# Kernel optimization log

Hardware: AMD Instinct MI355X
Metric: run time of the kernel (lower is better)

## Reference

```python
import jax, jax.numpy as jnp
import numpy as np

N_NODES = 50000
N_EDGES = 800000
NUM_GRAPHS = 256
EPS = 1e-5


def _gcn_conv(x, edge_index, W, b):
    # PyG GCNConv: add self-loops, sym-normalize, aggregate, then add bias.
    n = x.shape[0]
    xw = x @ W  # [N, out]
    loops = jnp.arange(n)
    row = jnp.concatenate([edge_index[0], loops])  # source
    col = jnp.concatenate([edge_index[1], loops])  # target
    deg = jax.ops.segment_sum(jnp.ones_like(col, dtype=xw.dtype), col, num_segments=n)
    dinv = jnp.where(deg > 0, jax.lax.rsqrt(deg), 0.0)
    norm = dinv[row] * dinv[col]  # [E+N]
    msg = norm[:, None] * xw[row]  # gather + scale
    out = jax.ops.segment_sum(msg, col, num_segments=n)  # scatter-add
    return out + b


def _bn(x, g, b, m, v):
    # inference-mode batch norm
    return (x - m) * jax.lax.rsqrt(v + EPS) * g + b


def reference(x, edge_index, batch, gcn_W0, gcn_b0, bn_g0, bn_b0, bn_m0, bn_v0,
              gcn_W1, gcn_b1, bn_g1, bn_b1, bn_m1, bn_v1,
              hW1, hb1, hg1, hbb1, hm1, hv1,
              hW2, hb2, hg2, hbb2, hm2, hv2,
              hW3, hb3, hW4, hb4):
    # GCN block 0
    h = _gcn_conv(x, edge_index, gcn_W0, gcn_b0)
    h = jax.nn.relu(_bn(h, bn_g0, bn_b0, bn_m0, bn_v0))  # dropout = identity (eval)
    # GCN block 1
    h = _gcn_conv(h, edge_index, gcn_W1, gcn_b1)
    h = jax.nn.relu(_bn(h, bn_g1, bn_b1, bn_m1, bn_v1))
    # global mean pool over graphs
    sums = jax.ops.segment_sum(h, batch, num_segments=NUM_GRAPHS)
    cnts = jax.ops.segment_sum(jnp.ones_like(batch, dtype=h.dtype), batch, num_segments=NUM_GRAPHS)
    pooled = sums / jnp.maximum(cnts, 1.0)[:, None]  # [G, 64]
    # MLP head (eval: dropout identity)
    z = jax.nn.relu(_bn(pooled @ hW1 + hb1, hg1, hbb1, hm1, hv1))
    z = jax.nn.relu(_bn(z @ hW2 + hb2, hg2, hbb2, hm2, hv2))
    z = jax.nn.relu(z @ hW3 + hb3)
    out = (z @ hW4 + hb4).reshape(-1)  # [G]
    return out


def setup_inputs() -> dict:
    key = jax.random.key(0)
    ks = jax.random.split(key, 12)
    d = 64
    inp = {
        'x': jax.random.normal(ks[0], (N_NODES, d), dtype=jnp.float32),
        'edge_index': jax.random.randint(ks[1], (2, N_EDGES), 0, N_NODES, dtype=jnp.int64),
        'batch': jnp.sort(jax.random.randint(ks[2], (N_NODES,), 0, NUM_GRAPHS, dtype=jnp.int64)),
        'gcn_W0': jax.random.normal(ks[3], (d, d), dtype=jnp.float32) * 0.1,
        'gcn_b0': jnp.zeros((d,), jnp.float32),
        'bn_g0': jnp.ones((d,), jnp.float32), 'bn_b0': jnp.zeros((d,), jnp.float32),
        'bn_m0': jnp.zeros((d,), jnp.float32), 'bn_v0': jnp.ones((d,), jnp.float32),
        'gcn_W1': jax.random.normal(ks[4], (d, d), dtype=jnp.float32) * 0.1,
        'gcn_b1': jnp.zeros((d,), jnp.float32),
        'bn_g1': jnp.ones((d,), jnp.float32), 'bn_b1': jnp.zeros((d,), jnp.float32),
        'bn_m1': jnp.zeros((d,), jnp.float32), 'bn_v1': jnp.ones((d,), jnp.float32),
        'hW1': jax.random.normal(ks[5], (d, 256), dtype=jnp.float32) * 0.1,
        'hb1': jnp.zeros((256,), jnp.float32),
        'hg1': jnp.ones((256,), jnp.float32), 'hbb1': jnp.zeros((256,), jnp.float32),
        'hm1': jnp.zeros((256,), jnp.float32), 'hv1': jnp.ones((256,), jnp.float32),
        'hW2': jax.random.normal(ks[6], (256, 128), dtype=jnp.float32) * 0.1,
        'hb2': jnp.zeros((128,), jnp.float32),
        'hg2': jnp.ones((128,), jnp.float32), 'hbb2': jnp.zeros((128,), jnp.float32),
        'hm2': jnp.zeros((128,), jnp.float32), 'hv2': jnp.ones((128,), jnp.float32),
        'hW3': jax.random.normal(ks[7], (128, 64), dtype=jnp.float32) * 0.1,
        'hb3': jnp.zeros((64,), jnp.float32),
        'hW4': jax.random.normal(ks[8], (64, 1), dtype=jnp.float32) * 0.1,
        'hb4': jnp.zeros((1,), jnp.float32),
    }
    return inp
```

## Files before the change

kernel.cpp:

```cpp
#include <hip/hip_runtime.h>
#include <hip/hip_bf16.h>
#include <hip/hip_fp16.h>

#define N_NODES 50000
#define N_EDGES 800000
#define NUM_GRAPHS 256
#define D 64
#define EPS 1e-5f
#define N_PART 8
#define PART_SIZE (N_NODES / N_PART)
#define SCAT_CHUNKS 512
#define WP 72

typedef _Float16 half8_t __attribute__((ext_vector_type(8)));
typedef float f32x4 __attribute__((ext_vector_type(4)));

__global__ __launch_bounds__(256) void scatter_cnt_kernel(
        const int* __restrict__ ei, int* __restrict__ cnt,
        unsigned short* __restrict__ ssrc, int cap, int E) {
    int p     = blockIdx.x & (N_PART - 1);
    int chunk = blockIdx.x >> 3;
    int per   = (E + SCAT_CHUNKS - 1) / SCAT_CHUNKS;
    int lo    = chunk * per;
    int hi    = lo + per; if (hi > E) hi = E;
    for (int e = lo + threadIdx.x; e < hi; e += 256) {
        int c = ei[E + e];
        if (c / PART_SIZE == p) {
            int r = ei[e];
            int pos = atomicAdd(&cnt[c], 1);
            if (pos < cap) ssrc[(size_t)c * cap + pos] = (unsigned short)r;
        }
    }
}

__global__ __launch_bounds__(256) void gemm64_kernel(const float* __restrict__ X,
                                                     const float* __restrict__ W,
                                                     const int* __restrict__ cnt,
                                                     __half* __restrict__ Yh, int N) {
    __shared__ _Float16 Xs[64 * WP];
    __shared__ _Float16 Wt[64 * WP];
    int tid  = threadIdx.x;
    int base = blockIdx.x * 64;
    for (int i = tid; i < 4096; i += 256) {
        int k = i >> 6, n = i & 63;
        Wt[n * WP + k] = (_Float16)W[i];
    }
    for (int i = tid; i < 1024; i += 256) {
        int r = i >> 4, c4 = (i & 15) * 4;
        float4 xv = (base + r < N)
            ? ((const float4*)X)[(size_t)(base + r) * 16 + (i & 15)]
            : make_float4(0.f, 0.f, 0.f, 0.f);
        _Float16* dst = &Xs[r * WP + c4];
        dst[0] = (_Float16)xv.x; dst[1] = (_Float16)xv.y;
        dst[2] = (_Float16)xv.z; dst[3] = (_Float16)xv.w;
    }
    __syncthreads();
    int wave  = tid >> 6;
    int lane  = tid & 63;
    int m     = lane & 15;
    int q     = lane >> 4;
    int row16 = wave * 16;
    half8_t a0 = *(const half8_t*)&Xs[(row16 + m) * WP + q * 8];
    half8_t a1 = *(const half8_t*)&Xs[(row16 + m) * WP + 32 + q * 8];
    f32x4 acc[4];
#pragma unroll
    for (int ct = 0; ct < 4; ct++) {
        half8_t b0 = *(const half8_t*)&Wt[(ct * 16 + m) * WP + q * 8];
        half8_t b1 = *(const half8_t*)&Wt[(ct * 16 + m) * WP + 32 + q * 8];
        f32x4 c = {0.f, 0.f, 0.f, 0.f};
        c = __builtin_amdgcn_mfma_f32_16x16x32_f16(a0, b0, c, 0, 0, 0);
        c = __builtin_amdgcn_mfma_f32_16x16x32_f16(a1, b1, c, 0, 0, 0);
        acc[ct] = c;
    }
    int   rows[4];
    float ws[4];
#pragma unroll
    for (int reg = 0; reg < 4; reg++) {
        rows[reg] = base + row16 + q * 4 + reg;
        ws[reg] = (rows[reg] < N) ? rsqrtf((float)cnt[rows[reg]] + 1.0f) : 0.0f;
    }
#pragma unroll
    for (int ct = 0; ct < 4; ct++) {
#pragma unroll
        for (int reg = 0; reg < 4; reg++) {
            if (rows[reg] < N)
                Yh[(size_t)rows[reg] * 64 + ct * 16 + m] =
                    (__half)(ws[reg] * acc[ct][reg]);
        }
    }
}

__device__ __forceinline__ void acc_row(uint4 v, float4& A, float4& B) {
    __half2* hp = (__half2*)&v;
    float2 q0 = __half22float2(hp[0]), q1 = __half22float2(hp[1]);
    float2 q2 = __half22float2(hp[2]), q3 = __half22float2(hp[3]);
    A.x += q0.x; A.y += q0.y; A.z += q1.x; A.w += q1.y;
    B.x += q2.x; B.y += q2.y; B.z += q3.x; B.w += q3.y;
}

__global__ __launch_bounds__(256) void agg_bn_kernel(
        const __half* __restrict__ xwh, const int* __restrict__ cnt,
        const unsigned short* __restrict__ ssrc, int cap,
        const float* __restrict__ b, const float* __restrict__ g,
        const float* __restrict__ bb, const float* __restrict__ m,
        const float* __restrict__ var,
        float* __restrict__ out, int N) {
    int gid  = blockIdx.x * blockDim.x + threadIdx.x;
    int lane = threadIdx.x & 63;
    int wave = gid >> 6;
    int grp  = lane >> 3;
    int f2   = lane & 7;
    int c = wave * 8 + grp;
    if (c >= N) return;
    const uint4* xw8 = (const uint4*)xwh;
    int n = cnt[c];
    if (n > cap) n = cap;
    float dc = rsqrtf((float)n + 1.0f);
    float4 accA = make_float4(0.f, 0.f, 0.f, 0.f);
    float4 accB = accA;
    acc_row(xw8[(size_t)c * 8 + f2], accA, accB);
    const unsigned short* idx = &ssrc[(size_t)c * cap];
    const uint4 z4 = make_uint4(0, 0, 0, 0);
    for (int e0 = 0; e0 < n; e0 += 4) {
        uint2 i4 = *(const uint2*)&idx[e0];
        int r0 = i4.x & 0xffff, r1 = i4.x >> 16;
        int r2 = i4.y & 0xffff, r3 = i4.y >> 16;
        uint4 v0 = (e0 + 0 < n) ? xw8[(size_t)r0 * 8 + f2] : z4;
        uint4 v1 = (e0 + 1 < n) ? xw8[(size_t)r1 * 8 + f2] : z4;
        uint4 v2 = (e0 + 2 < n) ? xw8[(size_t)r2 * 8 + f2] : z4;
        uint4 v3 = (e0 + 3 < n) ? xw8[(size_t)r3 * 8 + f2] : z4;
        acc_row(v0, accA, accB);
        acc_row(v1, accA, accB);
        acc_row(v2, accA, accB);
        acc_row(v3, accA, accB);
    }
#pragma unroll
    for (int half = 0; half < 2; half++) {
        int i4 = 2 * f2 + half;
        float4 acc = half ? accB : accA;
        float4 b4  = ((const float4*)b)[i4];
        float4 m4  = ((const float4*)m)[i4];
        float4 v4_ = ((const float4*)var)[i4];
        float4 g4  = ((const float4*)g)[i4];
        float4 bb4 = ((const float4*)bb)[i4];
        float4 h;
        h.x = (acc.x * dc + b4.x - m4.x) * (1.0f / sqrtf(v4_.x + EPS)) * g4.x + bb4.x;
        h.y = (acc.y * dc + b4.y - m4.y) * (1.0f / sqrtf(v4_.y + EPS)) * g4.y + bb4.y;
        h.z = (acc.z * dc + b4.z - m4.z) * (1.0f / sqrtf(v4_.z + EPS)) * g4.z + bb4.z;
        h.w = (acc.w * dc + b4.w - m4.w) * (1.0f / sqrtf(v4_.w + EPS)) * g4.w + bb4.w;
        h.x = h.x > 0.f ? h.x : 0.f;
        h.y = h.y > 0.f ? h.y : 0.f;
        h.z = h.z > 0.f ? h.z : 0.f;
        h.w = h.w > 0.f ? h.w : 0.f;
        ((float4*)out)[(size_t)c * 16 + i4] = h;
    }
}

__global__ __launch_bounds__(256) void pool_head_kernel(
        const float* __restrict__ h, const int* __restrict__ batch,
        const float* __restrict__ hW1, const float* __restrict__ hb1,
        const float* __restrict__ hg1, const float* __restrict__ hbb1,
        const float* __restrict__ hm1, const float* __restrict__ hv1,
        const float* __restrict__ hW2, const float* __restrict__ hb2,
        const float* __restrict__ hg2, const float* __restrict__ hbb2,
        const float* __restrict__ hm2, const float* __restrict__ hv2,
        const float* __restrict__ hW3, const float* __restrict__ hb3,
        const float* __restrict__ hW4, const float* __restrict__ hb4,
        float* __restrict__ out) {
    __shared__ int se[2];
    __shared__ float red[256];
    __shared__ float pooled[64];
    __shared__ float z1[256];
    __shared__ float z2[128];
    __shared__ float z3[64];
    int g = blockIdx.x;
    int t = threadIdx.x;
    if (t < 2) {
        int target = g + t;
        int lo = 0, hi = N_NODES;
        while (lo < hi) {
            int mid = (lo + hi) >> 1;
            if (batch[mid] < target) lo = mid + 1; else hi = mid;
        }
        se[t] = lo;
    }
    __syncthreads();
    int start = se[0], end = se[1];
    {
        int f = t & 63, rg = t >> 6;
        float part = 0.0f;
        for (int r = start + rg; r < end; r += 4) part += h[(size_t)r * 64 + f];
        red[t] = part;
        __syncthreads();
        if (t < 64) {
            float s = red[t] + red[t + 64] + red[t + 128] + red[t + 192];
            float cnt = (float)(end - start);
            cnt = cnt > 1.0f ? cnt : 1.0f;
            pooled[t] = s / cnt;
        }
    }
    __syncthreads();
    {
        float acc = hb1[t];
#pragma unroll
        for (int k = 0; k < 64; k++) acc += pooled[k] * hW1[k * 256 + t];
        acc = (acc - hm1[t]) * (1.0f / sqrtf(hv1[t] + EPS)) * hg1[t] + hbb1[t];
        z1[t] = acc > 0.0f ? acc : 0.0f;
    }
    __syncthreads();
    if (t < 128) {
        float acc = hb2[t];
#pragma unroll 8
        for (int k = 0; k < 256; k++) acc += z1[k] * hW2[k * 128 + t];
        acc = (acc - hm2[t]) * (1.0f / sqrtf(hv2[t] + EPS)) * hg2[t] + hbb2[t];
        z2[t] = acc > 0.0f ? acc : 0.0f;
    }
    __syncthreads();
    if (t < 64) {
        float acc = hb3[t];
#pragma unroll 8
        for (int k = 0; k < 128; k++) acc += z2[k] * hW3[k * 64 + t];
        z3[t] = acc > 0.0f ? acc : 0.0f;
    }
    __syncthreads();
    if (t < 64) {
        float v = z3[t] * hW4[t];
        for (int off = 32; off > 0; off >>= 1) v += __shfl_down(v, off, 64);
        if (t == 0) out[g] = v + hb4[0];
    }
}

extern "C" void kernel_launch(void* const* d_in, const int* in_sizes, int n_in,
                              void* d_out, int out_size, void* d_ws, size_t ws_size,
                              hipStream_t stream) {
    const float* x     = (const float*)d_in[0];
    const int*   ei    = (const int*)d_in[1];
    const int*   batch = (const int*)d_in[2];
    const float* W0 = (const float*)d_in[3];
    const float* b0 = (const float*)d_in[4];
    const float* g0 = (const float*)d_in[5];
    const float* bb0 = (const float*)d_in[6];
    const float* m0 = (const float*)d_in[7];
    const float* v0 = (const float*)d_in[8];
    const float* W1 = (const float*)d_in[9];
    const float* b1 = (const float*)d_in[10];
    const float* g1 = (const float*)d_in[11];
    const float* bb1 = (const float*)d_in[12];
    const float* m1 = (const float*)d_in[13];
    const float* v1 = (const float*)d_in[14];
    const float* hW1 = (const float*)d_in[15];
    const float* hb1 = (const float*)d_in[16];
    const float* hg1 = (const float*)d_in[17];
    const float* hbb1 = (const float*)d_in[18];
    const float* hm1 = (const float*)d_in[19];
    const float* hv1 = (const float*)d_in[20];
    const float* hW2 = (const float*)d_in[21];
    const float* hb2 = (const float*)d_in[22];
    const float* hg2 = (const float*)d_in[23];
    const float* hbb2 = (const float*)d_in[24];
    const float* hm2 = (const float*)d_in[25];
    const float* hv2 = (const float*)d_in[26];
    const float* hW3 = (const float*)d_in[27];
    const float* hb3 = (const float*)d_in[28];
    const float* hW4 = (const float*)d_in[29];
    const float* hb4 = (const float*)d_in[30];
    float* out = (float*)d_out;

    float*  bufA = (float*)d_ws;
    __half* xwh  = (__half*)bufA;
    float*  bufB = bufA + (size_t)N_NODES * D;
    int*    cnt  = (int*)(bufB + (size_t)N_NODES * D);
    unsigned short* ssrc = (unsigned short*)(cnt + N_NODES);

    size_t used  = ((size_t)2 * N_NODES * D + N_NODES) * 4;
    int cap = 64;
    if (ws_size >= used) {
        size_t avail = (ws_size - used) / ((size_t)N_NODES * 2);
        if (avail < (size_t)cap) cap = (int)avail & ~7;
    } else {
        cap = 0;
    }

    const int NT = 256;
    hipMemsetAsync(cnt, 0, (size_t)N_NODES * 4, stream);

    scatter_cnt_kernel<<<SCAT_CHUNKS * N_PART, NT, 0, stream>>>(ei, cnt, ssrc, cap, N_EDGES);

    int agg_blocks = ((N_NODES + 7) / 8 * 64 + NT - 1) / NT;
    gemm64_kernel<<<(N_NODES + 63) / 64, NT, 0, stream>>>(x, W0, cnt, xwh, N_NODES);
    agg_bn_kernel<<<agg_blocks, NT, 0, stream>>>(
        xwh, cnt, ssrc, cap, b0, g0, bb0, m0, v0, bufB, N_NODES);

    gemm64_kernel<<<(N_NODES + 63) / 64, NT, 0, stream>>>(bufB, W1, cnt, xwh, N_NODES);
    agg_bn_kernel<<<agg_blocks, NT, 0, stream>>>(
        xwh, cnt, ssrc, cap, b1, g1, bb1, m1, v1, bufB, N_NODES);

    pool_head_kernel<<<NUM_GRAPHS, NT, 0, stream>>>(bufB, batch,
        hW1, hb1, hg1, hbb1, hm1, hv1,
        hW2, hb2, hg2, hbb2, hm2, hv2,
        hW3, hb3, hW4, hb4, out);
}
```

Before: 267.6 us.

## Fuse first GEMM with edge scatter and move source-degree scaling into aggregation

The layer-0 GEMM no longer depends on degree counts. Its blocks are therefore merged into the scatter/count kernel as extra blocks, which removes one launch and lets the GEMM overlap with the atomic scatter. Each edge's source normalisation is now computed in the aggregation loop by reading cnt[r] and applying rsqrt. This adds a random 4-byte gather and a rsqrt per edge in both aggregation passes. The fused kernel carries GEMM shared memory in every block, which may reduce occupancy for the scatter blocks.

```diff
diff --git a/kernel.cpp b/kernel.cpp
--- a/kernel.cpp
+++ b/kernel.cpp
@@ -11,15 +11,73 @@
 #define PART_SIZE (N_NODES / N_PART)
 #define SCAT_CHUNKS 512
 #define WP 72
+#define GEMM_BLOCKS ((N_NODES + 63) / 64)
 
 typedef _Float16 half8_t __attribute__((ext_vector_type(8)));
 typedef float f32x4 __attribute__((ext_vector_type(4)));
 
-__global__ __launch_bounds__(256) void scatter_cnt_kernel(
+__device__ __forceinline__ void gemm_body(const float* __restrict__ X,
+                                          const float* __restrict__ W,
+                                          __half* __restrict__ Yh, int N,
+                                          int blk) {
+    __shared__ _Float16 Xs[64 * WP];
+    __shared__ _Float16 Wt[64 * WP];
+    int tid  = threadIdx.x;
+    int base = blk * 64;
+    for (int i = tid; i < 4096; i += 256) {
+        int k = i >> 6, n = i & 63;
+        Wt[n * WP + k] = (_Float16)W[i];
+    }
+    for (int i = tid; i < 1024; i += 256) {
+        int r = i >> 4, c4 = (i & 15) * 4;
+        float4 xv = (base + r < N)
+            ? ((const float4*)X)[(size_t)(base + r) * 16 + (i & 15)]
+            : make_float4(0.f, 0.f, 0.f, 0.f);
+        _Float16* dst = &Xs[r * WP + c4];
+        dst[0] = (_Float16)xv.x; dst[1] = (_Float16)xv.y;
+        dst[2] = (_Float16)xv.z; dst[3] = (_Float16)xv.w;
+    }
+    __syncthreads();
+    int wave  = tid >> 6;
+    int lane  = tid & 63;
+    int m     = lane & 15;
+    int q     = lane >> 4;
+    int row16 = wave * 16;
+    half8_t a0 = *(const half8_t*)&Xs[(row16 + m) * WP + q * 8];
+    half8_t a1 = *(const half8_t*)&Xs[(row16 + m) * WP + 32 + q * 8];
+    f32x4 acc[4];
+#pragma unroll
+    for (int ct = 0; ct < 4; ct++) {
+        half8_t b0 = *(const half8_t*)&Wt[(ct * 16 + m) * WP + q * 8];
+        half8_t b1 = *(const half8_t*)&Wt[(ct * 16 + m) * WP + 32 + q * 8];
+        f32x4 c = {0.f, 0.f, 0.f, 0.f};
+        c = __builtin_amdgcn_mfma_f32_16x16x32_f16(a0, b0, c, 0, 0, 0);
+        c = __builtin_amdgcn_mfma_f32_16x16x32_f16(a1, b1, c, 0, 0, 0);
+        acc[ct] = c;
+    }
+#pragma unroll
+    for (int ct = 0; ct < 4; ct++) {
+#pragma unroll
+        for (int reg = 0; reg < 4; reg++) {
+            int row = base + row16 + q * 4 + reg;
+            if (row < N)
+                Yh[(size_t)row * 64 + ct * 16 + m] = (__half)acc[ct][reg];
+        }
+    }
+}
+
+__global__ __launch_bounds__(256) void gemm_scatter_kernel(
+        const float* __restrict__ X, const float* __restrict__ W,
+        __half* __restrict__ Yh, int N,
         const int* __restrict__ ei, int* __restrict__ cnt,
         unsigned short* __restrict__ ssrc, int cap, int E) {
-    int p     = blockIdx.x & (N_PART - 1);
-    int chunk = blockIdx.x >> 3;
+    if (blockIdx.x < GEMM_BLOCKS) {
+        gemm_body(X, W, Yh, N, blockIdx.x);
+        return;
+    }
+    int b     = blockIdx.x - GEMM_BLOCKS;
+    int p     = b & (N_PART - 1);
+    int chunk = b >> 3;
     int per   = (E + SCAT_CHUNKS - 1) / SCAT_CHUNKS;
     int lo    = chunk * per;
     int hi    = lo + per; if (hi > E) hi = E;
@@ -35,67 +93,16 @@
 
 __global__ __launch_bounds__(256) void gemm64_kernel(const float* __restrict__ X,
                                                      const float* __restrict__ W,
-                                                     const int* __restrict__ cnt,
                                                      __half* __restrict__ Yh, int N) {
-    __shared__ _Float16 Xs[64 * WP];
-    __shared__ _Float16 Wt[64 * WP];
-    int tid  = threadIdx.x;
-    int base = blockIdx.x * 64;
-    for (int i = tid; i < 4096; i += 256) {
-        int k = i >> 6, n = i & 63;
-        Wt[n * WP + k] = (_Float16)W[i];
-    }
-    for (int i = tid; i < 1024; i += 256) {
-        int r = i >> 4, c4 = (i & 15) * 4;
-        float4 xv = (base + r < N)
-            ? ((const float4*)X)[(size_t)(base + r) * 16 + (i & 15)]
-            : make_float4(0.f, 0.f, 0.f, 0.f);
-        _Float16* dst = &Xs[r * WP + c4];
-        dst[0] = (_Float16)xv.x; dst[1] = (_Float16)xv.y;
-        dst[2] = (_Float16)xv.z; dst[3] = (_Float16)xv.w;
-    }
-    __syncthreads();
-    int wave  = tid >> 6;
-    int lane  = tid & 63;
-    int m     = lane & 15;
-    int q     = lane >> 4;
-    int row16 = wave * 16;
-    half8_t a0 = *(const half8_t*)&Xs[(row16 + m) * WP + q * 8];
-    half8_t a1 = *(const half8_t*)&Xs[(row16 + m) * WP + 32 + q * 8];
-    f32x4 acc[4];
-#pragma unroll
-    for (int ct = 0; ct < 4; ct++) {
-        half8_t b0 = *(const half8_t*)&Wt[(ct * 16 + m) * WP + q * 8];
-        half8_t b1 = *(const half8_t*)&Wt[(ct * 16 + m) * WP + 32 + q * 8];
-        f32x4 c = {0.f, 0.f, 0.f, 0.f};
-        c = __builtin_amdgcn_mfma_f32_16x16x32_f16(a0, b0, c, 0, 0, 0);
-        c = __builtin_amdgcn_mfma_f32_16x16x32_f16(a1, b1, c, 0, 0, 0);
-        acc[ct] = c;
-    }
-    int   rows[4];
-    float ws[4];
-#pragma unroll
-    for (int reg = 0; reg < 4; reg++) {
-        rows[reg] = base + row16 + q * 4 + reg;
-        ws[reg] = (rows[reg] < N) ? rsqrtf((float)cnt[rows[reg]] + 1.0f) : 0.0f;
-    }
-#pragma unroll
-    for (int ct = 0; ct < 4; ct++) {
-#pragma unroll
-        for (int reg = 0; reg < 4; reg++) {
-            if (rows[reg] < N)
-                Yh[(size_t)rows[reg] * 64 + ct * 16 + m] =
-                    (__half)(ws[reg] * acc[ct][reg]);
-        }
-    }
-}
-
-__device__ __forceinline__ void acc_row(uint4 v, float4& A, float4& B) {
+    gemm_body(X, W, Yh, N, blockIdx.x);
+}
+
+__device__ __forceinline__ void acc_roww(uint4 v, float w, float4& A, float4& B) {
     __half2* hp = (__half2*)&v;
     float2 q0 = __half22float2(hp[0]), q1 = __half22float2(hp[1]);
     float2 q2 = __half22float2(hp[2]), q3 = __half22float2(hp[3]);
-    A.x += q0.x; A.y += q0.y; A.z += q1.x; A.w += q1.y;
-    B.x += q2.x; B.y += q2.y; B.z += q3.x; B.w += q3.y;
+    A.x += w * q0.x; A.y += w * q0.y; A.z += w * q1.x; A.w += w * q1.y;
+    B.x += w * q2.x; B.y += w * q2.y; B.z += w * q3.x; B.w += w * q3.y;
 }
 
 __global__ __launch_bounds__(256) void agg_bn_kernel(
@@ -118,7 +125,7 @@
     float dc = rsqrtf((float)n + 1.0f);
     float4 accA = make_float4(0.f, 0.f, 0.f, 0.f);
     float4 accB = accA;
-    acc_row(xw8[(size_t)c * 8 + f2], accA, accB);
+    acc_roww(xw8[(size_t)c * 8 + f2], dc, accA, accB);
     const unsigned short* idx = &ssrc[(size_t)c * cap];
     const uint4 z4 = make_uint4(0, 0, 0, 0);
     for (int e0 = 0; e0 < n; e0 += 4) {
@@ -129,10 +136,14 @@
         uint4 v1 = (e0 + 1 < n) ? xw8[(size_t)r1 * 8 + f2] : z4;
         uint4 v2 = (e0 + 2 < n) ? xw8[(size_t)r2 * 8 + f2] : z4;
         uint4 v3 = (e0 + 3 < n) ? xw8[(size_t)r3 * 8 + f2] : z4;
-        acc_row(v0, accA, accB);
-        acc_row(v1, accA, accB);
-        acc_row(v2, accA, accB);
-        acc_row(v3, accA, accB);
+        float w0 = (e0 + 0 < n) ? rsqrtf((float)cnt[r0] + 1.0f) : 0.0f;
+        float w1 = (e0 + 1 < n) ? rsqrtf((float)cnt[r1] + 1.0f) : 0.0f;
+        float w2 = (e0 + 2 < n) ? rsqrtf((float)cnt[r2] + 1.0f) : 0.0f;
+        float w3 = (e0 + 3 < n) ? rsqrtf((float)cnt[r3] + 1.0f) : 0.0f;
+        acc_roww(v0, w0, accA, accB);
+        acc_roww(v1, w1, accA, accB);
+        acc_roww(v2, w2, accA, accB);
+        acc_roww(v3, w3, accA, accB);
     }
 #pragma unroll
     for (int half = 0; half < 2; half++) {
@@ -284,14 +295,14 @@
     const int NT = 256;
     hipMemsetAsync(cnt, 0, (size_t)N_NODES * 4, stream);
 
-    scatter_cnt_kernel<<<SCAT_CHUNKS * N_PART, NT, 0, stream>>>(ei, cnt, ssrc, cap, N_EDGES);
+    gemm_scatter_kernel<<<GEMM_BLOCKS + SCAT_CHUNKS * N_PART, NT, 0, stream>>>(
+        x, W0, xwh, N_NODES, ei, cnt, ssrc, cap, N_EDGES);
 
     int agg_blocks = ((N_NODES + 7) / 8 * 64 + NT - 1) / NT;
-    gemm64_kernel<<<(N_NODES + 63) / 64, NT, 0, stream>>>(x, W0, cnt, xwh, N_NODES);
     agg_bn_kernel<<<agg_blocks, NT, 0, stream>>>(
         xwh, cnt, ssrc, cap, b0, g0, bb0, m0, v0, bufB, N_NODES);
 
-    gemm64_kernel<<<(N_NODES + 63) / 64, NT, 0, stream>>>(bufB, W1, cnt, xwh, N_NODES);
+    gemm64_kernel<<<GEMM_BLOCKS, NT, 0, stream>>>(bufB, W1, xwh, N_NODES);
     agg_bn_kernel<<<agg_blocks, NT, 0, stream>>>(
         xwh, cnt, ssrc, cap, b1, g1, bb1, m1, v1, bufB, N_NODES);
 
```

After: 270.5 us. Within noise of the previous version (+1.1%).
